# Kernel tuning notes

Hardware: AMD Instinct MI355X
Metric: run time of the kernel (lower is better)

The kernel has to match this reference:

```python
import jax, jax.numpy as jnp
import numpy as np

# Bernstein-basis theta coefficients for d=2 (calculate_theta2(2)),
# inv_coeff order: [x^0, x^1, x^2]
THETAS = ((3.0, -3.0, 0.75), (0.0, 3.0, -1.5), (0.0, 0.0, 0.75))
HIGH_ORDER = 2

N_NODES = 50000
N_EDGES = 800000
IN_DIM, HID_DIM, OUT_DIM = 128, 64, 2


def setup_inputs() -> dict:
    key = jax.random.key(0)
    ks = jax.random.split(key, 16)
    f32 = jnp.float32
    def w(k, shape, fan_in):
        return jax.random.normal(k, shape, dtype=f32) * (1.0 / np.sqrt(fan_in))
    return {
        "in_feat": jax.random.normal(ks[0], (N_NODES, IN_DIM), dtype=f32),
        "src": jax.random.randint(ks[1], (N_EDGES,), 0, N_NODES, dtype=jnp.int32),
        "dst": jax.random.randint(ks[2], (N_EDGES,), 0, N_NODES, dtype=jnp.int32),
        "W1": w(ks[3], (IN_DIM, HID_DIM), IN_DIM), "b1": jnp.zeros((HID_DIM,), f32),
        "W2": w(ks[4], (HID_DIM, HID_DIM), HID_DIM), "b2": jnp.zeros((HID_DIM,), f32),
        "W3": w(ks[5], (HID_DIM * 5, HID_DIM), HID_DIM * 5), "b3": jnp.zeros((HID_DIM,), f32),
        "W4": w(ks[6], (HID_DIM, OUT_DIM), HID_DIM), "b4": jnp.zeros((OUT_DIM,), f32),
        "Wg1": w(ks[7], (IN_DIM, HID_DIM), IN_DIM), "bg1": jnp.zeros((HID_DIM,), f32),
        "Wg2": w(ks[8], (HID_DIM, IN_DIM), HID_DIM), "bg2": jnp.zeros((IN_DIM,), f32),
    }


def _spmm(x, src, dst, n):
    # y[v] = sum_{(u,v) in E} x[u]   (DGL update_all(copy_u, sum))
    return jax.ops.segment_sum(x[src], dst, num_segments=n)


def reference(in_feat, src, dst, W1, b1, W2, b2, W3, b3, W4, b4, Wg1, bg1, Wg2, bg2):
    n = in_feat.shape[0]
    ones_e = jnp.ones(src.shape[0], dtype=in_feat.dtype)
    deg_in = jnp.clip(jax.ops.segment_sum(ones_e, dst, num_segments=n), 1.0)
    deg_out = jnp.clip(jax.ops.segment_sum(ones_e, src, num_segments=n), 1.0)
    din = (deg_in ** -0.5)[:, None]   # [N,1]
    dout = (deg_out ** -0.5)[:, None]

    def lap(f):
        # f - D^{-1/2} A D^{-1/2} f  (in-degree norm, as in unnLaplacian)
        return f - _spmm(f * din, src, dst, n) * din

    # MLP front-end
    h = jax.nn.relu(in_feat @ W1 + b1)
    h = jax.nn.relu(h @ W2 + b2)

    branches = []
    # BandConv branches (lin=False): theta-weighted Laplacian polynomial
    for theta in THETAS:
        f = h
        acc = theta[0] * h
        for k in range(1, len(theta)):
            f = lap(f)
            acc = acc + theta[k] * f
        branches.append(acc)
    # HighConv branches: repeated Laplacian, num_layer = 1..HIGH_ORDER
    f = h
    for j in range(HIGH_ORDER):
        f = lap(f)
        branches.append(f)

    h_final = jnp.concatenate(branches, axis=-1)  # [N, 5*hid]
    out = jax.nn.relu(h_final @ W3 + b3) @ W4 + b4  # [N, out_dim]

    # GCN branch on self-loop-free graph (same edges here): symmetric norm GraphConv
    def gconv(x, W, b):
        return _spmm(x * dout, src, dst, n) * din @ W + b
    emb = gconv(jax.nn.relu(gconv(in_feat, Wg1, bg1)), Wg2, bg2)  # [N, in_dim]

    return out, emb
```

## Files before the change

### kernel.cpp

```cpp
#include <hip/hip_runtime.h>
#include <hip/hip_bf16.h>
#include <math.h>

#define NN 50000
#define NE 800000
#define C128 128
#define CE 6250
#define NR 8
#define RNOD 6250
#define RW 3125
#define NW 25000
#define HISTB 1024
#define INITB 96
#define RB 98
#define GB 782
#define ZSB 782
#define FSG 3125

typedef _Float16 half8 __attribute__((ext_vector_type(8)));
typedef float f32x4 __attribute__((ext_vector_type(4)));
typedef unsigned short ushort4v __attribute__((ext_vector_type(4)));

static inline int cdiv(int a, int b) { return (a + b - 1) / b; }


__device__ inline size_t pack_pos(int k, int n, int K, int M) {
    int tile = n >> 4;
    int kstep = k >> 5;
    int quad = (k >> 3) & 3;
    int j = k & 7;
    int lane = (quad << 4) | (n & 15);
    return ((size_t)(tile * (K >> 5) + kstep) * 64 + lane) * 8 + j;
}

__device__ void pack_std_dev(int bx, const float* __restrict__ W, _Float16* __restrict__ Wpk,
                             int K, int M) {
    int idx = bx * 256 + threadIdx.x;
    if (idx >= K * M) return;
    int k = idx / M, n = idx % M;
    Wpk[pack_pos(k, n, K, M)] = (_Float16)W[idx];
}

__device__ void pack_wc_dev(int bx, const float* __restrict__ W3, _Float16* __restrict__ wcpk) {
    int idx = bx * 256 + threadIdx.x;
    if (idx >= 3 * 4096) return;
    int b = idx >> 12;
    int rem = idx & 4095;
    int k = rem >> 6, n = rem & 63;
    float w0 = W3[(0 * 64 + k) * 64 + n];
    float w1 = W3[(1 * 64 + k) * 64 + n];
    float w2 = W3[(2 * 64 + k) * 64 + n];
    float w3 = W3[(3 * 64 + k) * 64 + n];
    float w4 = W3[(4 * 64 + k) * 64 + n];
    float v;
    if (b == 0)      v = 3.f * w0;
    else if (b == 1) v = -3.f * w0 + 3.f * w1 + w3;
    else             v = 0.75f * w0 - 1.5f * w1 + 0.75f * w2 + w4;
    wcpk[pack_pos(b * 64 + k, n, 192, 64)] = (_Float16)v;
}

__device__ void init_dev(int bx,
                         const float* __restrict__ W2, _Float16* __restrict__ W2pk,
                         const float* __restrict__ Wg2, _Float16* __restrict__ Wg2pk,
                         const float* __restrict__ W3, _Float16* __restrict__ wcpk) {
    if (bx < 16) { pack_std_dev(bx, W2, W2pk, 64, 64); return; }
    bx -= 16;
    if (bx < 32) { pack_std_dev(bx, Wg2, Wg2pk, 64, 128); return; }
    bx -= 32;
    pack_wc_dev(bx, W3, wcpk);
}


__device__ void hist_dev(int bx, const int* __restrict__ idx, unsigned* __restrict__ H,
                         unsigned* __restrict__ cnt) {
    int c = bx & 127, r = bx >> 7;
    int tid = threadIdx.x;
    for (int j = tid; j < RW; j += 256) cnt[j] = 0;
    __syncthreads();
    int lo = r * RNOD;
    const int2* p2 = (const int2*)(idx + (size_t)c * CE);
    for (int i = tid; i < CE / 2; i += 256) {
        int2 e = p2[i];
        int v0 = e.x - lo, v1 = e.y - lo;
        if ((unsigned)v0 < (unsigned)RNOD)
            atomicAdd(&cnt[v0 >> 1], 1u << ((v0 & 1) * 16));
        if ((unsigned)v1 < (unsigned)RNOD)
            atomicAdd(&cnt[v1 >> 1], 1u << ((v1 & 1) * 16));
    }
    __syncthreads();
    unsigned* outp = H + (size_t)c * NW + r * RW;
    for (int j = tid; j < RW; j += 256) outp[j] = cnt[j];
}

__device__ void reduce_dev(int bx, const unsigned* __restrict__ H,
                           float* __restrict__ o_rsq) {
    int w = bx * 256 + threadIdx.x;
    if (w >= NW) return;
    unsigned slo = 0, shi = 0;
#pragma unroll 8
    for (int c = 0; c < C128; c++) {
        unsigned h = H[(size_t)c * NW + w];
        slo += h & 0xffffu; shi += h >> 16;
    }
    float f0 = (float)(slo < 1u ? 1u : slo);
    float f1 = (float)(shi < 1u ? 1u : shi);
    o_rsq[2 * w] = rsqrtf(f0); o_rsq[2 * w + 1] = rsqrtf(f1);
}

__device__ void prefnorm_dev(int bx, const unsigned* __restrict__ HD,
                             unsigned* __restrict__ baseD,
                             int* __restrict__ dgo, float* __restrict__ o_rsq,
                             float* __restrict__ o_inv, float* __restrict__ o_sq) {
    int w = bx * 256 + threadIdx.x;
    if (w >= NW) return;
    unsigned slo = 0, shi = 0;
#pragma unroll 8
    for (int c = 0; c < C128; c++) {
        unsigned b0 = slo > 64u ? 64u : slo;
        unsigned b1 = shi > 64u ? 64u : shi;
        baseD[(size_t)c * NW + w] = b0 | (b1 << 16);
        unsigned h = HD[(size_t)c * NW + w];
        slo += h & 0xffffu; shi += h >> 16;
    }
    dgo[2 * w]     = slo > 64u ? 64 : (int)slo;
    dgo[2 * w + 1] = shi > 64u ? 64 : (int)shi;
    float f0 = (float)(slo < 1u ? 1u : slo);
    float f1 = (float)(shi < 1u ? 1u : shi);
    o_rsq[2 * w] = rsqrtf(f0); o_rsq[2 * w + 1] = rsqrtf(f1);
    o_inv[2 * w] = 1.f / f0;   o_inv[2 * w + 1] = 1.f / f1;
    o_sq[2 * w] = sqrtf(f0);   o_sq[2 * w + 1] = sqrtf(f1);
}

__device__ void scatter_dev(int bx, const int* __restrict__ src, const int* __restrict__ dst,
                            const unsigned* __restrict__ baseD,
                            unsigned short* __restrict__ colsPad,
                            unsigned* __restrict__ cnt) {
    int c = bx & 127, r = bx >> 7;
    int tid = threadIdx.x;
    const unsigned* bslice = baseD + (size_t)c * NW + r * RW;
    for (int j = tid; j < RW; j += 256) cnt[j] = bslice[j];
    __syncthreads();
    int lo = r * RNOD;
    const int2* pd2 = (const int2*)(dst + (size_t)c * CE);
    const int2* ps2 = (const int2*)(src + (size_t)c * CE);
    for (int i = tid; i < CE / 2; i += 256) {
        int2 ed = pd2[i];
        int2 es = ps2[i];
        int lv0 = ed.x - lo;
        if ((unsigned)lv0 < (unsigned)RNOD) {
            int sh = (lv0 & 1) * 16;
            unsigned old = atomicAdd(&cnt[lv0 >> 1], 1u << sh);
            unsigned pos = (old >> sh) & 0xffffu;
            if (pos < 64u) colsPad[(size_t)ed.x * 64 + pos] = (unsigned short)es.x;
        }
        int lv1 = ed.y - lo;
        if ((unsigned)lv1 < (unsigned)RNOD) {
            int sh = (lv1 & 1) * 16;
            unsigned old = atomicAdd(&cnt[lv1 >> 1], 1u << sh);
            unsigned pos = (old >> sh) & 0xffffu;
            if (pos < 64u) colsPad[(size_t)ed.y * 64 + pos] = (unsigned short)es.y;
        }
    }
}

__device__ void zscale_dev(int bx, half8* __restrict__ pair, const float* __restrict__ dout, int N) {
    int idx = bx * 256 + threadIdx.x;
    if (idx >= N * 4) return;
    int row = idx >> 2, q = idx & 3;
    float m = dout[row];
    half8* z = pair + (size_t)row * 16 + 8 + q * 2;
    half8 a = z[0], b = z[1];
#pragma unroll
    for (int j = 0; j < 8; j++) {
        a[j] = (_Float16)((float)a[j] * m);
        b[j] = (_Float16)((float)b[j] * m);
    }
    z[0] = a; z[1] = b;
}


struct HSegs { const _Float16* p[3]; int ld[3]; };

template <int M, int K, bool OUTW, bool RSCA>
__device__ void mg_dev(int bx, HSegs A, const half8* __restrict__ Wpk,
                       const float* __restrict__ bias, int relu,
                       float* __restrict__ C,
                       _Float16* __restrict__ Ch0, const float* __restrict__ ms0,
                       const float* __restrict__ rsc,
                       const float* __restrict__ W4, const float* __restrict__ b4,
                       float* __restrict__ outp, int ldC, int N) {
    constexpr int NT = M / 16;
    constexpr int NKS = K / 32;
    int tid = threadIdx.x;
    int wave = tid >> 6, lane = tid & 63;
    int quad = lane >> 4, m = lane & 15;
    int row0 = bx * 64 + wave * 16;
    int rowA = row0 + m; if (rowA >= N) rowA = N - 1;
    _Float16 hs = (_Float16)1.f;
    if (RSCA) hs = (_Float16)rsc[rowA];
    f32x4 acc[NT];
#pragma unroll
    for (int t = 0; t < NT; t++) acc[t] = (f32x4){0.f, 0.f, 0.f, 0.f};
#pragma unroll
    for (int ks = 0; ks < NKS; ks++) {
        const _Float16* ap = A.p[ks >> 1] + (size_t)rowA * A.ld[ks >> 1] + (ks & 1) * 32 + quad * 8;
        half8 af = *(const half8*)ap;
        if (RSCA) {
#pragma unroll
            for (int j = 0; j < 8; j++) af[j] *= hs;
        }
#pragma unroll
        for (int t = 0; t < NT; t++) {
            half8 bf = Wpk[(t * NKS + ks) * 64 + lane];
            acc[t] = __builtin_amdgcn_mfma_f32_16x16x32_f16(af, bf, acc[t], 0, 0, 0);
        }
    }
    float outv[NT][4];
#pragma unroll
    for (int t = 0; t < NT; t++) {
        float bv = bias ? bias[t * 16 + m] : 0.f;
#pragma unroll
        for (int r = 0; r < 4; r++) {
            float v = acc[t][r] + bv;
            if (relu) v = fmaxf(v, 0.f);
            outv[t][r] = v;
        }
    }
    if (OUTW) {
        float w40[NT], w41[NT];
#pragma unroll
        for (int t = 0; t < NT; t++) {
            w40[t] = W4[(t * 16 + m) * 2];
            w41[t] = W4[(t * 16 + m) * 2 + 1];
        }
#pragma unroll
        for (int r = 0; r < 4; r++) {
            float p0 = 0.f, p1 = 0.f;
#pragma unroll
            for (int t = 0; t < NT; t++) {
                p0 += outv[t][r] * w40[t];
                p1 += outv[t][r] * w41[t];
            }
#pragma unroll
            for (int off = 1; off < 16; off <<= 1) {
                p0 += __shfl_xor(p0, off);
                p1 += __shfl_xor(p1, off);
            }
            int row = row0 + quad * 4 + r;
            if (m == 0 && row < N) {
                outp[(size_t)row * 2 + 0] = p0 + b4[0];
                outp[(size_t)row * 2 + 1] = p1 + b4[1];
            }
        }
    }
    if (C || Ch0) {
#pragma unroll
        for (int r = 0; r < 4; r++) {
            int row = row0 + quad * 4 + r;
            if (row >= N) continue;
            float m0 = (Ch0 && ms0) ? ms0[row] : 1.f;
#pragma unroll
            for (int t = 0; t < NT; t++) {
                size_t off = (size_t)row * ldC + t * 16 + m;
                if (C)   C[off] = outv[t][r];
                if (Ch0) Ch0[off] = (_Float16)(outv[t][r] * m0);
            }
        }
    }
}

__device__ void a15_dev(int bx, const float* __restrict__ in_feat,
                        const float* __restrict__ W1, const float* __restrict__ Wg1,
                        const float* __restrict__ b1,
                        _Float16* __restrict__ h1h, _Float16* __restrict__ zh,
                        _Float16* __restrict__ wsm, int N) {
    int tid = threadIdx.x;
    int wave = tid >> 6, lane = tid & 63;
    int quad = lane >> 4, m = lane & 15;
    int row0 = bx * 64 + wave * 16;
    int rowA = row0 + m; if (rowA >= N) rowA = N - 1;
    half8 af[4];
#pragma unroll
    for (int ks = 0; ks < 4; ks++) {
        const float* ap = in_feat + (size_t)rowA * 128 + ks * 32 + quad * 8;
        float4 u = *(const float4*)ap;
        float4 v = *(const float4*)(ap + 4);
        af[ks][0] = (_Float16)u.x; af[ks][1] = (_Float16)u.y;
        af[ks][2] = (_Float16)u.z; af[ks][3] = (_Float16)u.w;
        af[ks][4] = (_Float16)v.x; af[ks][5] = (_Float16)v.y;
        af[ks][6] = (_Float16)v.z; af[ks][7] = (_Float16)v.w;
    }
    const half8* wf = (const half8*)wsm;
    f32x4 acc[4];
    for (int i = tid; i < 8192; i += 256)
        wsm[pack_pos(i >> 6, i & 63, 128, 64)] = (_Float16)W1[i];
    __syncthreads();
#pragma unroll
    for (int t = 0; t < 4; t++) acc[t] = (f32x4){0.f, 0.f, 0.f, 0.f};
#pragma unroll
    for (int ks = 0; ks < 4; ks++)
#pragma unroll
        for (int t = 0; t < 4; t++)
            acc[t] = __builtin_amdgcn_mfma_f32_16x16x32_f16(af[ks], wf[(t * 4 + ks) * 64 + lane], acc[t], 0, 0, 0);
#pragma unroll
    for (int r = 0; r < 4; r++) {
        int row = row0 + quad * 4 + r;
        if (row >= N) continue;
#pragma unroll
        for (int t = 0; t < 4; t++)
            h1h[(size_t)row * 64 + t * 16 + m] = (_Float16)fmaxf(acc[t][r] + b1[t * 16 + m], 0.f);
    }
    __syncthreads();
    for (int i = tid; i < 8192; i += 256)
        wsm[pack_pos(i >> 6, i & 63, 128, 64)] = (_Float16)Wg1[i];
    __syncthreads();
#pragma unroll
    for (int t = 0; t < 4; t++) acc[t] = (f32x4){0.f, 0.f, 0.f, 0.f};
#pragma unroll
    for (int ks = 0; ks < 4; ks++)
#pragma unroll
        for (int t = 0; t < 4; t++)
            acc[t] = __builtin_amdgcn_mfma_f32_16x16x32_f16(af[ks], wf[(t * 4 + ks) * 64 + lane], acc[t], 0, 0, 0);
#pragma unroll
    for (int r = 0; r < 4; r++) {
        int row = row0 + quad * 4 + r;
        if (row >= N) continue;
#pragma unroll
        for (int t = 0; t < 4; t++)
            zh[(size_t)row * 128 + t * 16 + m] = (_Float16)acc[t][r];
    }
}


__launch_bounds__(256)
__global__ void k_L1(const float* __restrict__ in_feat,
                     const float* __restrict__ W1, const float* __restrict__ Wg1,
                     const float* __restrict__ b1,
                     _Float16* __restrict__ h1h, _Float16* __restrict__ zh,
                     const int* __restrict__ src, const int* __restrict__ dst,
                     unsigned* __restrict__ HD, unsigned* __restrict__ HS, int N) {
    __shared__ _Float16 smh[8192];
    int bx = blockIdx.x;
    if (bx < GB) { a15_dev(bx, in_feat, W1, Wg1, b1, h1h, zh, smh, N); return; }
    bx -= GB;
    if (bx < HISTB) { hist_dev(bx, dst, HD, (unsigned*)smh); return; }
    bx -= HISTB;
    hist_dev(bx, src, HS, (unsigned*)smh);
}

__launch_bounds__(256)
__global__ void k_L2(const unsigned* __restrict__ HD, const unsigned* __restrict__ HS,
                     int* __restrict__ degin, float* __restrict__ din,
                     float* __restrict__ din2, float* __restrict__ dsq,
                     float* __restrict__ dout, unsigned* __restrict__ baseD,
                     const float* __restrict__ W2, _Float16* __restrict__ W2pk,
                     const float* __restrict__ Wg2, _Float16* __restrict__ Wg2pk,
                     const float* __restrict__ W3, _Float16* __restrict__ wcpk) {
    int bx = blockIdx.x;
    if (bx < RB) { reduce_dev(bx, HS, dout); return; }
    bx -= RB;
    if (bx < RB) { prefnorm_dev(bx, HD, baseD, degin, din, din2, dsq); return; }
    bx -= RB;
    init_dev(bx, W2, W2pk, Wg2, Wg2pk, W3, wcpk);
}

__launch_bounds__(256)
__global__ void k_L3(const int* __restrict__ src, const int* __restrict__ dst,
                     const unsigned* __restrict__ baseD, unsigned short* __restrict__ colsPad,
                     const _Float16* __restrict__ h1h, const half8* __restrict__ W2pk,
                     const float* __restrict__ b2, _Float16* __restrict__ pair0h,
                     const float* __restrict__ din,
                     half8* __restrict__ pair0v, const float* __restrict__ dout, int N) {
    __shared__ unsigned cnt[RW];
    int bx = blockIdx.x;
    if (bx < HISTB) { scatter_dev(bx, src, dst, baseD, colsPad, cnt); return; }
    bx -= HISTB;
    if (bx < GB) {
        HSegs A;
        A.p[0] = h1h; A.ld[0] = 64;
        A.p[1] = nullptr; A.ld[1] = 0;
        A.p[2] = nullptr; A.ld[2] = 0;
        mg_dev<64, 64, false, false>(bx, A, W2pk, b2, 1, nullptr, pair0h, din,
                                     nullptr, nullptr, nullptr, nullptr, 128, N);
        return;
    }
    bx -= GB;
    zscale_dev(bx, pair0v, dout, N);
}


struct FSP {
    const half8* xp;
    half8* uOut; int uld;
    half8* zOut; int zld;
    const float* din2;
    const float* zrs1;
    const float* bgz;
    const float* zrs2;
    int zrelu;
};

__launch_bounds__(256)
__global__ void k_FS(FSP P, const unsigned short* __restrict__ colsPad,
                     const int* __restrict__ deg, int N) {
    int g = blockIdx.x;
    int tid = threadIdx.x;
    int wave = tid >> 6, lane = tid & 63;
    int grp = lane >> 4, c = lane & 15;
    int row = g * 16 + wave * 4 + grp;
    if (row >= N) return;
    int dg = deg[row];
    const unsigned short* cp = colsPad + (size_t)row * 64;
    float acc[8];
#pragma unroll
    for (int j = 0; j < 8; j++) acc[j] = 0.f;
    int e = 0;
    for (; e + 7 < dg; e += 8) {
        ushort4v sa = *(const ushort4v*)(cp + e);
        ushort4v sb = *(const ushort4v*)(cp + e + 4);
        half8 v0 = P.xp[(size_t)sa.x * 16 + c];
        half8 v1 = P.xp[(size_t)sa.y * 16 + c];
        half8 v2 = P.xp[(size_t)sa.z * 16 + c];
        half8 v3 = P.xp[(size_t)sa.w * 16 + c];
        half8 v4 = P.xp[(size_t)sb.x * 16 + c];
        half8 v5 = P.xp[(size_t)sb.y * 16 + c];
        half8 v6 = P.xp[(size_t)sb.z * 16 + c];
        half8 v7 = P.xp[(size_t)sb.w * 16 + c];
#pragma unroll
        for (int j = 0; j < 8; j++) {
            acc[j] += (float)v0[j] + (float)v1[j] + (float)v2[j] + (float)v3[j]
                    + (float)v4[j] + (float)v5[j] + (float)v6[j] + (float)v7[j];
        }
    }
    for (; e + 3 < dg; e += 4) {
        ushort4v ss = *(const ushort4v*)(cp + e);
        half8 v0 = P.xp[(size_t)ss.x * 16 + c];
        half8 v1 = P.xp[(size_t)ss.y * 16 + c];
        half8 v2 = P.xp[(size_t)ss.z * 16 + c];
        half8 v3 = P.xp[(size_t)ss.w * 16 + c];
#pragma unroll
        for (int j = 0; j < 8; j++)
            acc[j] += (float)v0[j] + (float)v1[j] + (float)v2[j] + (float)v3[j];
    }
    for (; e < dg; e++) {
        int s = cp[e];
        half8 v = P.xp[(size_t)s * 16 + c];
#pragma unroll
        for (int j = 0; j < 8; j++) acc[j] += (float)v[j];
    }
    half8 h;
    if (c < 8) {
        float d = P.din2[row];
        half8 f = P.xp[(size_t)row * 16 + c];
#pragma unroll
        for (int j = 0; j < 8; j++)
            h[j] = (_Float16)((float)f[j] - acc[j] * d);
        P.uOut[(size_t)row * P.uld + c] = h;
    } else {
        float s1 = P.zrs1[row];
#pragma unroll
        for (int j = 0; j < 8; j++) acc[j] *= s1;
        if (P.bgz) {
            const float* bb = P.bgz + (c - 8) * 8;
#pragma unroll
            for (int j = 0; j < 8; j++) acc[j] += bb[j];
        }
        if (P.zrelu) {
#pragma unroll
            for (int j = 0; j < 8; j++) acc[j] = fmaxf(acc[j], 0.f);
        }
        float s2 = P.zrs2 ? P.zrs2[row] : 1.f;
#pragma unroll
        for (int j = 0; j < 8; j++) h[j] = (_Float16)(acc[j] * s2);
        P.zOut[(size_t)row * P.zld + (c - 8)] = h;
    }
}

__launch_bounds__(256)
__global__ void k_F3(const _Float16* __restrict__ pair0, const _Float16* __restrict__ pair1,
                     const _Float16* __restrict__ u2h, const half8* __restrict__ wcpk,
                     const float* __restrict__ b3, const float* __restrict__ dsq,
                     const float* __restrict__ W4, const float* __restrict__ b4,
                     float* __restrict__ outp,
                     const _Float16* __restrict__ sgh, const half8* __restrict__ Wg2pk,
                     const float* __restrict__ bg2, float* __restrict__ emb, int N) {
    int bx = blockIdx.x;
    if (bx < GB) {
        HSegs A;
        A.p[0] = pair0; A.ld[0] = 128;
        A.p[1] = pair1; A.ld[1] = 128;
        A.p[2] = u2h;   A.ld[2] = 64;
        mg_dev<64, 192, true, true>(bx, A, wcpk, b3, 1, nullptr, nullptr, nullptr,
                                    dsq, W4, b4, outp, 64, N);
        return;
    }
    bx -= GB;
    HSegs A;
    A.p[0] = sgh; A.ld[0] = 64;
    A.p[1] = nullptr; A.ld[1] = 0;
    A.p[2] = nullptr; A.ld[2] = 0;
    mg_dev<128, 64, false, false>(bx, A, Wg2pk, bg2, 0, emb, nullptr, nullptr,
                                  nullptr, nullptr, nullptr, nullptr, 128, N);
}

extern "C" void kernel_launch(void* const* d_in, const int* in_sizes, int n_in,
                              void* d_out, int out_size, void* d_ws, size_t ws_size,
                              hipStream_t stream) {
    const int N = NN;
    const float* in_feat = (const float*)d_in[0];
    const int* src = (const int*)d_in[1];
    const int* dst = (const int*)d_in[2];
    const float* W1 = (const float*)d_in[3];
    const float* b1 = (const float*)d_in[4];
    const float* W2 = (const float*)d_in[5];
    const float* b2 = (const float*)d_in[6];
    const float* W3 = (const float*)d_in[7];
    const float* b3 = (const float*)d_in[8];
    const float* W4 = (const float*)d_in[9];
    const float* b4 = (const float*)d_in[10];
    const float* Wg1 = (const float*)d_in[11];
    const float* bg1 = (const float*)d_in[12];
    const float* Wg2 = (const float*)d_in[13];
    const float* bg2 = (const float*)d_in[14];

    float* out = (float*)d_out;
    float* emb = out + (size_t)N * 2;

    float* fw = (float*)d_ws;
    float* din  = fw;
    float* din2 = din + N;
    float* dsq  = din2 + N;
    float* dout = dsq + N;
    int* degin  = (int*)(dout + N);
    unsigned short* colsPad = (unsigned short*)(degin + N);
    unsigned* HD   = (unsigned*)(colsPad + (size_t)64 * N);
    unsigned* HS   = HD + (size_t)C128 * NW;
    unsigned* baseD = HS + (size_t)C128 * NW;
    _Float16* hp = (_Float16*)(baseD + (size_t)C128 * NW);
    _Float16* h1h   = hp;
    _Float16* pair0 = h1h + (size_t)64 * N;
    _Float16* pair1 = pair0 + (size_t)128 * N;
    _Float16* u2h   = pair1 + (size_t)128 * N;
    _Float16* sgh   = u2h + (size_t)64 * N;
    _Float16* W2pk  = sgh + (size_t)64 * N;
    _Float16* Wg2pk = W2pk + 4096;
    _Float16* wcpk  = Wg2pk + 8192;

    k_L1<<<GB + 2 * HISTB, 256, 0, stream>>>(in_feat, W1, Wg1, b1,
        h1h, pair0 + 64, src, dst, HD, HS, N);

    k_L2<<<2 * RB + INITB, 256, 0, stream>>>(HD, HS, degin, din, din2, dsq, dout, baseD,
        W2, W2pk, Wg2, Wg2pk, W3, wcpk);

    k_L3<<<HISTB + GB + ZSB, 256, 0, stream>>>(src, dst, baseD, colsPad,
        h1h, (const half8*)W2pk, b2, pair0, din, (half8*)pair0, dout, N);

    FSP p;
    p = {(const half8*)pair0, (half8*)pair1, 16, (half8*)pair1 + 8, 16,
         din2, din, bg1, dout, 1};
    k_FS<<<FSG, 256, 0, stream>>>(p, colsPad, degin, N);

    p = {(const half8*)pair1, (half8*)u2h, 8, (half8*)sgh, 8,
         din2, din, nullptr, nullptr, 0};
    k_FS<<<FSG, 256, 0, stream>>>(p, colsPad, degin, N);

    k_F3<<<2 * GB, 256, 0, stream>>>(pair0, pair1, u2h, (const half8*)wcpk, b3, dsq,
        W4, b4, out, sgh, (const half8*)Wg2pk, bg2, emb, N);
}
```

Before: 240.0 us.

## Split each row's edge gather across four lane groups with shuffle reduction

```diff
diff --git a/kernel.cpp b/kernel.cpp
--- a/kernel.cpp
+++ b/kernel.cpp
@@ -15,7 +15,7 @@
 #define RB 98
 #define GB 782
 #define ZSB 782
-#define FSG 3125
+#define FSB 12500
 
 typedef _Float16 half8 __attribute__((ext_vector_type(8)));
 typedef float f32x4 __attribute__((ext_vector_type(4)));
@@ -403,51 +403,47 @@
 __launch_bounds__(256)
 __global__ void k_FS(FSP P, const unsigned short* __restrict__ colsPad,
                      const int* __restrict__ deg, int N) {
-    int g = blockIdx.x;
     int tid = threadIdx.x;
     int wave = tid >> 6, lane = tid & 63;
-    int grp = lane >> 4, c = lane & 15;
-    int row = g * 16 + wave * 4 + grp;
+    int row = blockIdx.x * 4 + wave;
     if (row >= N) return;
     int dg = deg[row];
+    int c = lane & 15;
+    int esub = lane >> 4;
     const unsigned short* cp = colsPad + (size_t)row * 64;
     float acc[8];
 #pragma unroll
     for (int j = 0; j < 8; j++) acc[j] = 0.f;
     int e = 0;
     for (; e + 7 < dg; e += 8) {
-        ushort4v sa = *(const ushort4v*)(cp + e);
-        ushort4v sb = *(const ushort4v*)(cp + e + 4);
-        half8 v0 = P.xp[(size_t)sa.x * 16 + c];
-        half8 v1 = P.xp[(size_t)sa.y * 16 + c];
-        half8 v2 = P.xp[(size_t)sa.z * 16 + c];
-        half8 v3 = P.xp[(size_t)sa.w * 16 + c];
-        half8 v4 = P.xp[(size_t)sb.x * 16 + c];
-        half8 v5 = P.xp[(size_t)sb.y * 16 + c];
-        half8 v6 = P.xp[(size_t)sb.z * 16 + c];
-        half8 v7 = P.xp[(size_t)sb.w * 16 + c];
-#pragma unroll
-        for (int j = 0; j < 8; j++) {
-            acc[j] += (float)v0[j] + (float)v1[j] + (float)v2[j] + (float)v3[j]
-                    + (float)v4[j] + (float)v5[j] + (float)v6[j] + (float)v7[j];
-        }
+        int s0 = cp[e + esub];
+        int s1 = cp[e + 4 + esub];
+        half8 v0 = P.xp[(size_t)s0 * 16 + c];
+        half8 v1 = P.xp[(size_t)s1 * 16 + c];
+#pragma unroll
+        for (int j = 0; j < 8; j++) acc[j] += (float)v0[j] + (float)v1[j];
     }
     for (; e + 3 < dg; e += 4) {
-        ushort4v ss = *(const ushort4v*)(cp + e);
-        half8 v0 = P.xp[(size_t)ss.x * 16 + c];
-        half8 v1 = P.xp[(size_t)ss.y * 16 + c];
-        half8 v2 = P.xp[(size_t)ss.z * 16 + c];
-        half8 v3 = P.xp[(size_t)ss.w * 16 + c];
-#pragma unroll
-        for (int j = 0; j < 8; j++)
-            acc[j] += (float)v0[j] + (float)v1[j] + (float)v2[j] + (float)v3[j];
-    }
-    for (; e < dg; e++) {
-        int s = cp[e];
-        half8 v = P.xp[(size_t)s * 16 + c];
-#pragma unroll
-        for (int j = 0; j < 8; j++) acc[j] += (float)v[j];
-    }
+        int s0 = cp[e + esub];
+        half8 v0 = P.xp[(size_t)s0 * 16 + c];
+#pragma unroll
+        for (int j = 0; j < 8; j++) acc[j] += (float)v0[j];
+    }
+    if (e < dg) {
+        int idx = e + esub;
+        if (idx < dg) {
+            int s0 = cp[idx];
+            half8 v0 = P.xp[(size_t)s0 * 16 + c];
+#pragma unroll
+            for (int j = 0; j < 8; j++) acc[j] += (float)v0[j];
+        }
+    }
+#pragma unroll
+    for (int j = 0; j < 8; j++) {
+        acc[j] += __shfl_xor(acc[j], 16);
+        acc[j] += __shfl_xor(acc[j], 32);
+    }
+    if (lane >= 16) return;
     half8 h;
     if (c < 8) {
         float d = P.din2[row];
@@ -558,11 +554,11 @@
     FSP p;
     p = {(const half8*)pair0, (half8*)pair1, 16, (half8*)pair1 + 8, 16,
          din2, din, bg1, dout, 1};
-    k_FS<<<FSG, 256, 0, stream>>>(p, colsPad, degin, N);
+    k_FS<<<FSB, 256, 0, stream>>>(p, colsPad, degin, N);
 
     p = {(const half8*)pair1, (half8*)u2h, 8, (half8*)sgh, 8,
          din2, din, nullptr, nullptr, 0};
-    k_FS<<<FSG, 256, 0, stream>>>(p, colsPad, degin, N);
+    k_FS<<<FSB, 256, 0, stream>>>(p, colsPad, degin, N);
 
     k_F3<<<2 * GB, 256, 0, stream>>>(pair0, pair1, u2h, (const half8*)wcpk, b3, dsq,
         W4, b4, out, sgh, (const half8*)Wg2pk, bg2, emb, N);
```

New measurement: 239.6 us. About the same (-0.1%).
